# Optimization experiments

Measured on AMD Instinct MI355X. Metric: run time of the kernel, lower is better.

## Reference

```python
import jax, jax.numpy as jnp
import numpy as np

N, F, C, H = 6144, 128, 64, 4
NEG = -1.0e10


def setup_inputs() -> dict:
    key = jax.random.key(0)
    ks = jax.random.split(key, 8)
    X = jax.random.normal(ks[0], (N, F), dtype=jnp.float32)
    A = (jax.random.uniform(ks[1], (N, N)) < 0.01).astype(jnp.float32)  # sparse-ish 0/1 adjacency
    A = A.at[jnp.arange(N), jnp.arange(N)].set(1.0)  # self loops so every row has a neighbor
    s = 1.0 / np.sqrt(F)
    W1 = jax.random.normal(ks[2], (H, F, C), dtype=jnp.float32) * s
    W2 = jax.random.normal(ks[3], (H, F, C), dtype=jnp.float32) * s
    a_self = jax.random.normal(ks[4], (H, C), dtype=jnp.float32) * (1.0 / np.sqrt(C))
    a_neigh = jax.random.normal(ks[5], (H, C), dtype=jnp.float32) * (1.0 / np.sqrt(C))
    bias = jnp.zeros((H, C), dtype=jnp.float32)
    return {"X": X, "A": A, "W1": W1, "W2": W2, "a_self": a_self, "a_neigh": a_neigh, "bias": bias}


def reference(X, A, W1, W2, a_self, a_neigh, bias):
    # Per-head projections: [H, N, C]
    feats = jnp.einsum('nf,hfc->hnc', X, W1)
    feats2 = jnp.einsum('nf,hfc->hnc', X, W2)
    # Attention logits: self term + transposed neighbor term -> [H, N, N]
    att_s = jnp.einsum('hnc,hc->hn', feats, a_self)
    att_n = jnp.einsum('hnc,hc->hn', feats, a_neigh)
    dense = att_s[:, :, None] + att_n[:, None, :]
    dense = jnp.where(dense > 0, dense, 0.2 * dense)  # LeakyReLU(0.2)
    dense = dense + NEG * (1.0 - A)[None, :, :]       # additive adjacency mask
    attn = jax.nn.softmax(dense, axis=-1)
    # Dropout layers are identity at inference.
    node = jnp.einsum('hnm,hmc->hnc', attn, feats) + feats2 + bias[:, None, :]
    out = jnp.mean(node, axis=0)  # attn_heads_reduction='average'
    return jax.nn.relu(out)
```

## Files before the change

### kernel.cpp

```cpp
#include <hip/hip_runtime.h>
#include <hip/hip_bf16.h>


#define N_NODES 6144
#define F_DIM   128
#define C_DIM   64
#define H_HEADS 4
#define MAXK    512

__global__ __launch_bounds__(256) void proj_kernel(
    const float* __restrict__ X,
    const float* __restrict__ W1, const float* __restrict__ W2,
    const float* __restrict__ a_self, const float* __restrict__ a_neigh,
    float* __restrict__ feats, float* __restrict__ feats2,
    float* __restrict__ att_s, float* __restrict__ att_n)
{
    const int rt    = blockIdx.x;
    const int z     = blockIdx.y;
    const int h     = z >> 1;
    const int which = z & 1;

    const float* W   = (which ? W2 : W1) + h * F_DIM * C_DIM;
    float*       out = (which ? feats2 : feats) + (size_t)h * N_NODES * C_DIM;

    __shared__ float Xs[64][132];
    __shared__ float Ws[128][68];

    const int tid = threadIdx.x;

    {
        const float4* Xg = (const float4*)(X + (size_t)rt * 64 * F_DIM);
        for (int u = tid; u < 64 * 32; u += 256) {
            const int r = u >> 5, q = u & 31;
            *(float4*)&Xs[r][4 * q] = Xg[u];
        }
        const float4* Wg = (const float4*)W;
        for (int u = tid; u < 128 * 16; u += 256) {
            const int k = u >> 4, q = u & 15;
            *(float4*)&Ws[k][4 * q] = Wg[u];
        }
    }
    __syncthreads();

    const int tx = tid & 15;
    const int ty = tid >> 4;

    float acc[4][4] = {};
    #pragma unroll 4
    for (int k = 0; k < 128; ++k) {
        const float4 b = *(const float4*)&Ws[k][tx * 4];
        const float a0 = Xs[ty * 4 + 0][k];
        const float a1 = Xs[ty * 4 + 1][k];
        const float a2 = Xs[ty * 4 + 2][k];
        const float a3 = Xs[ty * 4 + 3][k];
        acc[0][0] += a0 * b.x; acc[0][1] += a0 * b.y; acc[0][2] += a0 * b.z; acc[0][3] += a0 * b.w;
        acc[1][0] += a1 * b.x; acc[1][1] += a1 * b.y; acc[1][2] += a1 * b.z; acc[1][3] += a1 * b.w;
        acc[2][0] += a2 * b.x; acc[2][1] += a2 * b.y; acc[2][2] += a2 * b.z; acc[2][3] += a2 * b.w;
        acc[3][0] += a3 * b.x; acc[3][1] += a3 * b.y; acc[3][2] += a3 * b.z; acc[3][3] += a3 * b.w;
    }

    __syncthreads();
    float* Ct = &Xs[0][0];

    #pragma unroll
    for (int i = 0; i < 4; ++i) {
        const int r = 4 * ty + i;
        float4 v = make_float4(acc[i][0], acc[i][1], acc[i][2], acc[i][3]);
        *(float4*)&out[(size_t)(rt * 64 + r) * C_DIM + 4 * tx] = v;
        if (which == 0) {
            Ct[r * 65 + 4 * tx + 0] = acc[i][0];
            Ct[r * 65 + 4 * tx + 1] = acc[i][1];
            Ct[r * 65 + 4 * tx + 2] = acc[i][2];
            Ct[r * 65 + 4 * tx + 3] = acc[i][3];
        }
    }

    if (which == 0) {
        __syncthreads();
        if (tid < 64) {
            const float* as_ = a_self  + h * C_DIM;
            const float* an_ = a_neigh + h * C_DIM;
            float s = 0.f, n = 0.f;
            #pragma unroll 8
            for (int c = 0; c < C_DIM; ++c) {
                const float v = Ct[tid * 65 + c];
                s += v * as_[c];
                n += v * an_[c];
            }
            att_s[h * N_NODES + rt * 64 + tid] = s;
            att_n[h * N_NODES + rt * 64 + tid] = n;
        }
    }
}

__global__ __launch_bounds__(256) void agg_kernel(
    const float* __restrict__ A,
    const float* __restrict__ feats, const float* __restrict__ feats2,
    const float* __restrict__ att_s, const float* __restrict__ att_n,
    const float* __restrict__ bias,
    float* __restrict__ out)
{
    const int i   = blockIdx.x;
    const int tid = threadIdx.x;

    __shared__ int   idx[MAXK];
    __shared__ int   cnt;
    __shared__ float ew[H_HEADS][MAXK];
    __shared__ float mh[H_HEADS], Zh[H_HEADS], si[H_HEADS];
    __shared__ float nodebuf[256];

    if (tid == 0) cnt = 0;
    if (tid < H_HEADS) si[tid] = att_s[tid * N_NODES + i];
    __syncthreads();

    const float4* Arow = (const float4*)(A + (size_t)i * N_NODES);
    for (int u = tid; u < N_NODES / 4; u += 256) {
        const float4 v = Arow[u];
        if (v.x > 0.5f) { int p = atomicAdd(&cnt, 1); if (p < MAXK) idx[p] = 4 * u + 0; }
        if (v.y > 0.5f) { int p = atomicAdd(&cnt, 1); if (p < MAXK) idx[p] = 4 * u + 1; }
        if (v.z > 0.5f) { int p = atomicAdd(&cnt, 1); if (p < MAXK) idx[p] = 4 * u + 2; }
        if (v.w > 0.5f) { int p = atomicAdd(&cnt, 1); if (p < MAXK) idx[p] = 4 * u + 3; }
    }
    __syncthreads();
    const int K = min(cnt, MAXK);

    for (int k = tid; k < K; k += 256) {
        const int j = idx[k];
        #pragma unroll
        for (int h = 0; h < H_HEADS; ++h) {
            float l = si[h] + att_n[h * N_NODES + j];
            l = (l > 0.f) ? l : 0.2f * l;
            ew[h][k] = l;
        }
    }
    __syncthreads();

    const int w    = tid >> 6;
    const int lane = tid & 63;

    {
        float m = -1e30f;
        for (int k = lane; k < K; k += 64) m = fmaxf(m, ew[w][k]);
        #pragma unroll
        for (int off = 32; off > 0; off >>= 1) m = fmaxf(m, __shfl_down(m, off));
        if (lane == 0) mh[w] = m;
    }
    __syncthreads();

    {
        const float m = mh[w];
        float zsum = 0.f;
        for (int k = lane; k < K; k += 64) {
            const float e = __expf(ew[w][k] - m);
            ew[w][k] = e;
            zsum += e;
        }
        #pragma unroll
        for (int off = 32; off > 0; off >>= 1) zsum += __shfl_down(zsum, off);
        if (lane == 0) Zh[w] = zsum;
    }
    __syncthreads();

    const int h = w, c = lane;
    const float* fh = feats + (size_t)h * N_NODES * C_DIM + c;
    float acc = 0.f;
    for (int k = 0; k < K; ++k) {
        acc += ew[h][k] * fh[(size_t)idx[k] * C_DIM];
    }
    const float node = acc / Zh[h]
                     + feats2[((size_t)h * N_NODES + i) * C_DIM + c]
                     + bias[h * C_DIM + c];
    nodebuf[tid] = node;
    __syncthreads();

    if (tid < 64) {
        const float s = nodebuf[tid] + nodebuf[64 + tid] + nodebuf[128 + tid] + nodebuf[192 + tid];
        out[(size_t)i * C_DIM + tid] = fmaxf(0.25f * s, 0.f);
    }
}

extern "C" void kernel_launch(void* const* d_in, const int* in_sizes, int n_in,
                              void* d_out, int out_size, void* d_ws, size_t ws_size,
                              hipStream_t stream) {
    const float* X       = (const float*)d_in[0];
    const float* A       = (const float*)d_in[1];
    const float* W1      = (const float*)d_in[2];
    const float* W2      = (const float*)d_in[3];
    const float* a_self  = (const float*)d_in[4];
    const float* a_neigh = (const float*)d_in[5];
    const float* bias    = (const float*)d_in[6];
    float* out = (float*)d_out;

    float* ws     = (float*)d_ws;
    float* feats  = ws;
    float* feats2 = feats  + (size_t)H_HEADS * N_NODES * C_DIM;
    float* att_s  = feats2 + (size_t)H_HEADS * N_NODES * C_DIM;
    float* att_n  = att_s  + (size_t)H_HEADS * N_NODES;

    dim3 grid1(N_NODES / 64, H_HEADS * 2);
    proj_kernel<<<grid1, 256, 0, stream>>>(X, W1, W2, a_self, a_neigh,
                                           feats, feats2, att_s, att_n);

    agg_kernel<<<N_NODES, 256, 0, stream>>>(A, feats, feats2, att_s, att_n, bias, out);
}
```

Before: 269.7 us.

## Store projections node-major and unroll neighbor gather in aggregation

Projected features and attention terms are now written node-major ([N, H*C] and [N, H]), so each aggregation block gathers one contiguous 1 KB row per neighbor across all heads and reads the four neighbor logits as a single float4. The gather loop is unrolled by 8 with vectorized index and weight loads from shared memory, giving more independent loads in flight. The projection GEMM inner loop is also reworked to read X as float4 and reuse four W rows per step. Cost: the projection store is strided by head, and the unrolled loop uses more registers.

New measurement: 266.3 us. Within noise of the previous version (-1.3%).

```diff
diff --git a/kernel.cpp b/kernel.cpp
--- a/kernel.cpp
+++ b/kernel.cpp
@@ -6,25 +6,26 @@
 #define F_DIM   128
 #define C_DIM   64
 #define H_HEADS 4
+#define HC      (H_HEADS * C_DIM)
 #define MAXK    512
 
 __global__ __launch_bounds__(256) void proj_kernel(
     const float* __restrict__ X,
     const float* __restrict__ W1, const float* __restrict__ W2,
     const float* __restrict__ a_self, const float* __restrict__ a_neigh,
-    float* __restrict__ feats, float* __restrict__ feats2,
-    float* __restrict__ att_s, float* __restrict__ att_n)
+    float* __restrict__ featsT, float* __restrict__ feats2T,
+    float* __restrict__ attsT, float* __restrict__ attnT)
 {
     const int rt    = blockIdx.x;
     const int z     = blockIdx.y;
     const int h     = z >> 1;
     const int which = z & 1;
 
-    const float* W   = (which ? W2 : W1) + h * F_DIM * C_DIM;
-    float*       out = (which ? feats2 : feats) + (size_t)h * N_NODES * C_DIM;
-
-    __shared__ float Xs[64][132];
-    __shared__ float Ws[128][68];
+    const float* W    = (which ? W2 : W1) + h * F_DIM * C_DIM;
+    float*       outp = which ? feats2T : featsT;
+
+    __shared__ float  Xs[64][132];
+    __shared__ float4 Ws4[128][17];
 
     const int tid = threadIdx.x;
 
@@ -36,8 +37,7 @@
         }
         const float4* Wg = (const float4*)W;
         for (int u = tid; u < 128 * 16; u += 256) {
-            const int k = u >> 4, q = u & 15;
-            *(float4*)&Ws[k][4 * q] = Wg[u];
+            Ws4[u >> 4][u & 15] = Wg[u];
         }
     }
     __syncthreads();
@@ -46,17 +46,19 @@
     const int ty = tid >> 4;
 
     float acc[4][4] = {};
-    #pragma unroll 4
-    for (int k = 0; k < 128; ++k) {
-        const float4 b = *(const float4*)&Ws[k][tx * 4];
-        const float a0 = Xs[ty * 4 + 0][k];
-        const float a1 = Xs[ty * 4 + 1][k];
-        const float a2 = Xs[ty * 4 + 2][k];
-        const float a3 = Xs[ty * 4 + 3][k];
-        acc[0][0] += a0 * b.x; acc[0][1] += a0 * b.y; acc[0][2] += a0 * b.z; acc[0][3] += a0 * b.w;
-        acc[1][0] += a1 * b.x; acc[1][1] += a1 * b.y; acc[1][2] += a1 * b.z; acc[1][3] += a1 * b.w;
-        acc[2][0] += a2 * b.x; acc[2][1] += a2 * b.y; acc[2][2] += a2 * b.z; acc[2][3] += a2 * b.w;
-        acc[3][0] += a3 * b.x; acc[3][1] += a3 * b.y; acc[3][2] += a3 * b.z; acc[3][3] += a3 * b.w;
+    for (int k = 0; k < 128; k += 4) {
+        const float4 b0 = Ws4[k + 0][tx];
+        const float4 b1 = Ws4[k + 1][tx];
+        const float4 b2 = Ws4[k + 2][tx];
+        const float4 b3 = Ws4[k + 3][tx];
+        #pragma unroll
+        for (int i = 0; i < 4; ++i) {
+            const float4 x = *(const float4*)&Xs[4 * ty + i][k];
+            acc[i][0] += x.x * b0.x + x.y * b1.x + x.z * b2.x + x.w * b3.x;
+            acc[i][1] += x.x * b0.y + x.y * b1.y + x.z * b2.y + x.w * b3.y;
+            acc[i][2] += x.x * b0.z + x.y * b1.z + x.z * b2.z + x.w * b3.z;
+            acc[i][3] += x.x * b0.w + x.y * b1.w + x.z * b2.w + x.w * b3.w;
+        }
     }
 
     __syncthreads();
@@ -64,9 +66,10 @@
 
     #pragma unroll
     for (int i = 0; i < 4; ++i) {
-        const int r = 4 * ty + i;
-        float4 v = make_float4(acc[i][0], acc[i][1], acc[i][2], acc[i][3]);
-        *(float4*)&out[(size_t)(rt * 64 + r) * C_DIM + 4 * tx] = v;
+        const int r    = 4 * ty + i;
+        const int node = rt * 64 + r;
+        *(float4*)&outp[(size_t)node * HC + h * C_DIM + 4 * tx] =
+            make_float4(acc[i][0], acc[i][1], acc[i][2], acc[i][3]);
         if (which == 0) {
             Ct[r * 65 + 4 * tx + 0] = acc[i][0];
             Ct[r * 65 + 4 * tx + 1] = acc[i][1];
@@ -87,16 +90,17 @@
                 s += v * as_[c];
                 n += v * an_[c];
             }
-            att_s[h * N_NODES + rt * 64 + tid] = s;
-            att_n[h * N_NODES + rt * 64 + tid] = n;
+            const int node = rt * 64 + tid;
+            attsT[node * H_HEADS + h] = s;
+            attnT[node * H_HEADS + h] = n;
         }
     }
 }
 
 __global__ __launch_bounds__(256) void agg_kernel(
     const float* __restrict__ A,
-    const float* __restrict__ feats, const float* __restrict__ feats2,
-    const float* __restrict__ att_s, const float* __restrict__ att_n,
+    const float* __restrict__ featsT, const float* __restrict__ feats2T,
+    const float* __restrict__ attsT, const float* __restrict__ attnT,
     const float* __restrict__ bias,
     float* __restrict__ out)
 {
@@ -104,13 +108,13 @@
     const int tid = threadIdx.x;
 
     __shared__ int   idx[MAXK];
+    __shared__ float ews[H_HEADS][MAXK];
     __shared__ int   cnt;
-    __shared__ float ew[H_HEADS][MAXK];
     __shared__ float mh[H_HEADS], Zh[H_HEADS], si[H_HEADS];
     __shared__ float nodebuf[256];
 
     if (tid == 0) cnt = 0;
-    if (tid < H_HEADS) si[tid] = att_s[tid * N_NODES + i];
+    if (tid < H_HEADS) si[tid] = attsT[i * H_HEADS + tid];
     __syncthreads();
 
     const float4* Arow = (const float4*)(A + (size_t)i * N_NODES);
@@ -124,14 +128,14 @@
     __syncthreads();
     const int K = min(cnt, MAXK);
 
+    const float4* an4 = (const float4*)attnT;
     for (int k = tid; k < K; k += 256) {
-        const int j = idx[k];
-        #pragma unroll
-        for (int h = 0; h < H_HEADS; ++h) {
-            float l = si[h] + att_n[h * N_NODES + j];
-            l = (l > 0.f) ? l : 0.2f * l;
-            ew[h][k] = l;
-        }
+        const float4 an = an4[idx[k]];
+        float l;
+        l = si[0] + an.x; ews[0][k] = (l > 0.f) ? l : 0.2f * l;
+        l = si[1] + an.y; ews[1][k] = (l > 0.f) ? l : 0.2f * l;
+        l = si[2] + an.z; ews[2][k] = (l > 0.f) ? l : 0.2f * l;
+        l = si[3] + an.w; ews[3][k] = (l > 0.f) ? l : 0.2f * l;
     }
     __syncthreads();
 
@@ -140,7 +144,7 @@
 
     {
         float m = -1e30f;
-        for (int k = lane; k < K; k += 64) m = fmaxf(m, ew[w][k]);
+        for (int k = lane; k < K; k += 64) m = fmaxf(m, ews[w][k]);
         #pragma unroll
         for (int off = 32; off > 0; off >>= 1) m = fmaxf(m, __shfl_down(m, off));
         if (lane == 0) mh[w] = m;
@@ -151,8 +155,8 @@
         const float m = mh[w];
         float zsum = 0.f;
         for (int k = lane; k < K; k += 64) {
-            const float e = __expf(ew[w][k] - m);
-            ew[w][k] = e;
+            const float e = __expf(ews[w][k] - m);
+            ews[w][k] = e;
             zsum += e;
         }
         #pragma unroll
@@ -162,14 +166,30 @@
     __syncthreads();
 
     const int h = w, c = lane;
-    const float* fh = feats + (size_t)h * N_NODES * C_DIM + c;
+    const float* fh = featsT + h * C_DIM + c;
     float acc = 0.f;
-    for (int k = 0; k < K; ++k) {
-        acc += ew[h][k] * fh[(size_t)idx[k] * C_DIM];
-    }
+    int k = 0;
+    for (; k + 8 <= K; k += 8) {
+        const int4   j0 = *(const int4*)&idx[k];
+        const int4   j1 = *(const int4*)&idx[k + 4];
+        const float4 w0 = *(const float4*)&ews[h][k];
+        const float4 w1 = *(const float4*)&ews[h][k + 4];
+        const float f0 = fh[(size_t)j0.x * HC];
+        const float f1 = fh[(size_t)j0.y * HC];
+        const float f2 = fh[(size_t)j0.z * HC];
+        const float f3 = fh[(size_t)j0.w * HC];
+        const float f4 = fh[(size_t)j1.x * HC];
+        const float f5 = fh[(size_t)j1.y * HC];
+        const float f6 = fh[(size_t)j1.z * HC];
+        const float f7 = fh[(size_t)j1.w * HC];
+        acc += w0.x * f0 + w0.y * f1 + w0.z * f2 + w0.w * f3
+             + w1.x * f4 + w1.y * f5 + w1.z * f6 + w1.w * f7;
+    }
+    for (; k < K; ++k) acc += ews[h][k] * fh[(size_t)idx[k] * HC];
+
     const float node = acc / Zh[h]
-                     + feats2[((size_t)h * N_NODES + i) * C_DIM + c]
-                     + bias[h * C_DIM + c];
+                     + feats2T[(size_t)i * HC + tid]
+                     + bias[tid];
     nodebuf[tid] = node;
     __syncthreads();
 
@@ -191,15 +211,15 @@
     const float* bias    = (const float*)d_in[6];
     float* out = (float*)d_out;
 
-    float* ws     = (float*)d_ws;
-    float* feats  = ws;
-    float* feats2 = feats  + (size_t)H_HEADS * N_NODES * C_DIM;
-    float* att_s  = feats2 + (size_t)H_HEADS * N_NODES * C_DIM;
-    float* att_n  = att_s  + (size_t)H_HEADS * N_NODES;
+    float* ws      = (float*)d_ws;
+    float* featsT  = ws;
+    float* feats2T = featsT  + (size_t)N_NODES * HC;
+    float* attsT   = feats2T + (size_t)N_NODES * HC;
+    float* attnT   = attsT   + (size_t)N_NODES * H_HEADS;
 
     dim3 grid1(N_NODES / 64, H_HEADS * 2);
     proj_kernel<<<grid1, 256, 0, stream>>>(X, W1, W2, a_self, a_neigh,
-                                           feats, feats2, att_s, att_n);
-
-    agg_kernel<<<N_NODES, 256, 0, stream>>>(A, feats, feats2, att_s, att_n, bias, out);
+                                           featsT, feats2T, attsT, attnT);
+
+    agg_kernel<<<N_NODES, 256, 0, stream>>>(A, featsT, feats2T, attsT, attnT, bias, out);
 }
```
